# Kernel tuning notes

Measured on AMD Instinct MI355X. Metric: run time of the kernel, lower is better.

Reference implementation:

```python
import jax, jax.numpy as jnp
import numpy as np

T_STEPS = 64   # number of actions (T-1 in the torch code)
BATCH = 512
STATE = 256
ACTION = 64
BELIEF = 1024
HIDDEN = 1024
EMB = 1024
MIN_STD = 0.1


def setup_inputs() -> dict:
    key = jax.random.key(0)
    ks = jax.random.split(key, 16)
    def w(k, shape):
        return jax.random.normal(k, shape, jnp.float32) * 0.02
    return {
        "s_0": jax.random.normal(ks[0], (BATCH, STATE), jnp.float32),
        "A": jax.random.normal(ks[1], (T_STEPS, BATCH, ACTION), jnp.float32),
        "b_0": jax.random.normal(ks[2], (BATCH, BELIEF), jnp.float32),
        "O": jax.random.normal(ks[3], (T_STEPS, BATCH, EMB), jnp.float32),
        "M": jnp.ones((T_STEPS, BATCH, 1), jnp.float32),
        "noise_pri": jax.random.normal(ks[4], (T_STEPS, BATCH, STATE), jnp.float32),
        "noise_pos": jax.random.normal(ks[5], (T_STEPS, BATCH, STATE), jnp.float32),
        # learned parameters (torch nn.Linear convention: y = x @ W.T + b)
        "W_sa": w(ks[6], (BELIEF, STATE + ACTION)), "b_sa": jnp.zeros((BELIEF,), jnp.float32),
        "W_ih": w(ks[7], (3 * BELIEF, BELIEF)), "b_ih": jnp.zeros((3 * BELIEF,), jnp.float32),
        "W_hh": w(ks[8], (3 * BELIEF, BELIEF)), "b_hh": jnp.zeros((3 * BELIEF,), jnp.float32),
        "W_bpri": w(ks[9], (HIDDEN, BELIEF)), "b_bpri": jnp.zeros((HIDDEN,), jnp.float32),
        "W_spri": w(ks[10], (2 * STATE, HIDDEN)), "b_spri": jnp.zeros((2 * STATE,), jnp.float32),
        "W_bpos": w(ks[11], (HIDDEN, BELIEF + EMB)), "b_bpos": jnp.zeros((HIDDEN,), jnp.float32),
        "W_spos": w(ks[12], (2 * STATE, HIDDEN)), "b_spos": jnp.zeros((2 * STATE,), jnp.float32),
    }


def reference(s_0, A, b_0, O, M, noise_pri, noise_pos,
              W_sa, b_sa, W_ih, b_ih, W_hh, b_hh,
              W_bpri, b_bpri, W_spri, b_spri,
              W_bpos, b_bpos, W_spos, b_spos):
    act = jax.nn.relu  # cfg.activation_function = 'relu'

    def gru_cell(x, h):
        # torch GRUCell gate order: r, z, n
        gi = x @ W_ih.T + b_ih      # [B, 3*BELIEF]
        gh = h @ W_hh.T + b_hh
        i_r, i_z, i_n = jnp.split(gi, 3, axis=1)
        h_r, h_z, h_n = jnp.split(gh, 3, axis=1)
        r = jax.nn.sigmoid(i_r + h_r)
        z = jax.nn.sigmoid(i_z + h_z)
        n = jnp.tanh(i_n + r * h_n)
        return (1.0 - z) * n + z * h

    def step(carry, xs):
        b, s = carry  # belief [B,BELIEF], posterior state [B,STATE]
        a_t, o_t, m_t, eps_p, eps_q = xs
        s_in = s * m_t  # non-terminal mask
        x = act(jnp.concatenate([s_in, a_t], axis=1) @ W_sa.T + b_sa)
        b_new = gru_cell(x, b)
        # prior
        pri = act(b_new @ W_bpri.T + b_bpri) @ W_spri.T + b_spri
        mu_p, hp = jnp.split(pri, 2, axis=1)
        std_p = jax.nn.softplus(hp) + MIN_STD
        s_p = mu_p + std_p * eps_p
        # posterior (uses current observation embedding)
        pos = act(jnp.concatenate([b_new, o_t], axis=1) @ W_bpos.T + b_bpos) @ W_spos.T + b_spos
        mu_q, hq = jnp.split(pos, 2, axis=1)
        std_q = jax.nn.softplus(hq) + MIN_STD
        s_q = mu_q + std_q * eps_q
        return (b_new, s_q), (b_new, s_p, mu_p, std_p, s_q, mu_q, std_q)

    (_, _), ys = jax.lax.scan(step, (b_0, s_0), (A, O, M, noise_pri, noise_pos))
    B_out, S_pri, MU_pri, STD_pri, S_pos, MU_pos, STD_pos = ys
    return B_out, S_pri, MU_pri, STD_pri, S_pos, MU_pos, STD_pos
```

## Files before the change

kernel.cpp:

```cpp
#include <hip/hip_runtime.h>
#include <hip/hip_bf16.h>
#include <math.h>

typedef short bf16x8 __attribute__((ext_vector_type(8)));
typedef float f32x4 __attribute__((ext_vector_type(4)));
typedef unsigned short u16;

#define NT 64
#define NB 512
#define NS 256
#define NA 64
#define NBEL 1024

#define OUT_B      0
#define OUT_SPRI   33554432
#define OUT_MUPRI  41943040
#define OUT_STDPRI 50331648
#define OUT_SPOS   58720256
#define OUT_MUPOS  67108864
#define OUT_STDPOS 75497472

__device__ __forceinline__ f32x4 mfma16(bf16x8 a, bf16x8 b, f32x4 c) {
  return __builtin_amdgcn_mfma_f32_16x16x32_bf16(a, b, c, 0, 0, 0);
}

__device__ __forceinline__ u16 f2bf(float f) {
  union { float f; unsigned u; } v; v.f = f;
  return (u16)((v.u + 0x7FFFu + ((v.u >> 16) & 1u)) >> 16);
}

__device__ __forceinline__ bf16x8 ld8bf(const u16* p) { return *(const bf16x8*)p; }

__device__ __forceinline__ bf16x8 cvt8(const float* p) {
  const float4 lo = *(const float4*)p;
  const float4 hi = *(const float4*)(p + 4);
  bf16x8 v;
  v[0] = (short)f2bf(lo.x); v[1] = (short)f2bf(lo.y);
  v[2] = (short)f2bf(lo.z); v[3] = (short)f2bf(lo.w);
  v[4] = (short)f2bf(hi.x); v[5] = (short)f2bf(hi.y);
  v[6] = (short)f2bf(hi.z); v[7] = (short)f2bf(hi.w);
  return v;
}

__device__ __forceinline__ float sigm(float x) { return 1.f / (1.f + __expf(-x)); }
__device__ __forceinline__ float softplus_(float x) {
  if (x > 20.f) return x;
  return log1pf(__expf(x));
}

#define ZACC(acc) { acc[0][0] = (f32x4){0.f,0.f,0.f,0.f}; acc[0][1] = (f32x4){0.f,0.f,0.f,0.f}; \
                    acc[1][0] = (f32x4){0.f,0.f,0.f,0.f}; acc[1][1] = (f32x4){0.f,0.f,0.f,0.f}; }

#define Q4(acc, a0v, a1v, b0v, b1v) \
  acc[0][0] = mfma16(a0v, b0v, acc[0][0]); \
  acc[0][1] = mfma16(a0v, b1v, acc[0][1]); \
  acc[1][0] = mfma16(a1v, b0v, acc[1][0]); \
  acc[1][1] = mfma16(a1v, b1v, acc[1][1]);

__device__ __forceinline__ void red_write(float* L, f32x4 (&acc)[2][2], int l) {
  const int base = l * 16;
#pragma unroll
  for (int i = 0; i < 2; ++i)
#pragma unroll
    for (int j = 0; j < 2; ++j)
#pragma unroll
      for (int q = 0; q < 4; ++q)
        L[base + (i * 2 + j) * 4 + q] = acc[i][j][q];
}
__device__ __forceinline__ void red_add(const float* L, f32x4 (&acc)[2][2], int l) {
  const int base = l * 16;
#pragma unroll
  for (int i = 0; i < 2; ++i)
#pragma unroll
    for (int j = 0; j < 2; ++j)
#pragma unroll
      for (int q = 0; q < 4; ++q)
        acc[i][j][q] += L[base + (i * 2 + j) * 4 + q];
}

__global__ __launch_bounds__(256) void cvt_weights_k(
    const float* __restrict__ wsa, const float* __restrict__ wih,
    const float* __restrict__ whh, const float* __restrict__ wbpri,
    const float* __restrict__ wspri, const float* __restrict__ wbpos,
    const float* __restrict__ wspos, u16* __restrict__ dst) {
  const int S0 = 327680;
  const int S1 = S0 + 3145728;
  const int S2 = S1 + 3145728;
  const int S3 = S2 + 1048576;
  const int S4 = S3 + 524288;
  const int S5 = S4 + 2097152;
  const int S6 = S5 + 524288;
  for (int i = blockIdx.x * blockDim.x + threadIdx.x; i < S6;
       i += gridDim.x * blockDim.x) {
    float v;
    if (i < S0) v = wsa[i];
    else if (i < S1) v = wih[i - S0];
    else if (i < S2) v = whh[i - S1];
    else if (i < S3) v = wbpri[i - S2];
    else if (i < S4) v = wspri[i - S3];
    else if (i < S5) v = wbpos[i - S4];
    else v = wspos[i - S5];
    dst[i] = f2bf(v);
  }
}

__global__ __launch_bounds__(256) void init_carry_k(
    const float* __restrict__ s0, const float* __restrict__ b0,
    const float* __restrict__ Mptr, u16* __restrict__ smask,
    u16* __restrict__ bbf0, float* __restrict__ hf) {
  for (int i = blockIdx.x * blockDim.x + threadIdx.x; i < NB * NBEL;
       i += gridDim.x * blockDim.x) {
    float b = b0[i];
    bbf0[i] = f2bf(b);
    hf[i] = b;
    if (i < NB * NS) {
      int row = i >> 8;
      smask[i] = f2bf(s0[i] * Mptr[row]);
    }
  }
}

__global__ __launch_bounds__(512, 2) void kA(
    const u16* __restrict__ smask, const float* __restrict__ Af,
    const u16* __restrict__ wsa, const float* __restrict__ bsa,
    u16* __restrict__ xbf, const float* __restrict__ Of,
    const u16* __restrict__ wbpos, float* __restrict__ hbO, int t) {
  __shared__ float lred[4][1024];
  const int l = threadIdx.x & 63, r16 = l & 15, kq = l >> 4;
  const int wid8 = threadIdx.x >> 6;
  const int wid = wid8 & 3, kh = wid8 >> 2;
  if (blockIdx.x < 128) {
    const int g = blockIdx.x, bm = g >> 4, bn = g & 15;
    const int row0 = bm * 64 + (wid >> 1) * 32;
    const int col0 = bn * 64 + (wid & 1) * 32;
    f32x4 acc[2][2]; ZACC(acc);
    const u16* A0 = smask + (row0 + r16) * NS + kq * 8;
    const u16* A1 = A0 + 16 * NS;
    const u16* B0 = wsa + (size_t)(col0 + r16) * 320 + kq * 8;
    const u16* B1 = B0 + 16 * 320;
    if (kh == 0) {
#pragma unroll
      for (int k = 0; k < 160; k += 32) {
        bf16x8 a0 = ld8bf(A0 + k), a1 = ld8bf(A1 + k);
        bf16x8 b0 = ld8bf(B0 + k), b1 = ld8bf(B1 + k);
        Q4(acc, a0, a1, b0, b1);
      }
    } else {
#pragma unroll
      for (int k = 160; k < 256; k += 32) {
        bf16x8 a0 = ld8bf(A0 + k), a1 = ld8bf(A1 + k);
        bf16x8 b0 = ld8bf(B0 + k), b1 = ld8bf(B1 + k);
        Q4(acc, a0, a1, b0, b1);
      }
      const float* F0 = Af + (size_t)t * (NB * NA) + (row0 + r16) * NA + kq * 8;
      const float* F1 = F0 + 16 * NA;
      const u16* C0 = wsa + (size_t)(col0 + r16) * 320 + 256 + kq * 8;
      const u16* C1 = C0 + 16 * 320;
#pragma unroll
      for (int k = 0; k < 64; k += 32) {
        bf16x8 a0 = cvt8(F0 + k), a1 = cvt8(F1 + k);
        bf16x8 b0 = ld8bf(C0 + k), b1 = ld8bf(C1 + k);
        Q4(acc, a0, a1, b0, b1);
      }
      red_write(lred[wid], acc, l);
    }
    __syncthreads();
    if (kh == 0) {
      red_add(lred[wid], acc, l);
#pragma unroll
      for (int i = 0; i < 2; ++i)
#pragma unroll
        for (int j = 0; j < 2; ++j)
#pragma unroll
          for (int q = 0; q < 4; ++q) {
            const int row = row0 + i * 16 + kq * 4 + q;
            const int col = col0 + j * 16 + r16;
            xbf[row * NBEL + col] = f2bf(fmaxf(acc[i][j][q] + bsa[col], 0.f));
          }
    }
  } else {
    const int g = blockIdx.x - 128, bm = g >> 4, bn = g & 15;
    const int row0 = bm * 64 + (wid >> 1) * 32;
    const int col0 = bn * 64 + (wid & 1) * 32;
    f32x4 acc[2][2]; ZACC(acc);
    const float* F0 = Of + (size_t)t * (NB * NBEL) + (row0 + r16) * NBEL + kh * 512 + kq * 8;
    const float* F1 = F0 + 16 * NBEL;
    const u16* B0 = wbpos + (size_t)(col0 + r16) * 2048 + 1024 + kh * 512 + kq * 8;
    const u16* B1 = B0 + 16 * 2048;
#pragma unroll 4
    for (int k = 0; k < 512; k += 32) {
      bf16x8 a0 = cvt8(F0 + k), a1 = cvt8(F1 + k);
      bf16x8 b0 = ld8bf(B0 + k), b1 = ld8bf(B1 + k);
      Q4(acc, a0, a1, b0, b1);
    }
    if (kh == 1) red_write(lred[wid], acc, l);
    __syncthreads();
    if (kh == 0) {
      red_add(lred[wid], acc, l);
#pragma unroll
      for (int i = 0; i < 2; ++i)
#pragma unroll
        for (int j = 0; j < 2; ++j)
#pragma unroll
          for (int q = 0; q < 4; ++q) {
            const int row = row0 + i * 16 + kq * 4 + q;
            const int col = col0 + j * 16 + r16;
            hbO[row * NBEL + col] = acc[i][j][q];
          }
    }
  }
}

__global__ __launch_bounds__(512, 2) void kB(
    const u16* __restrict__ xbf, const u16* __restrict__ bprev,
    const u16* __restrict__ wih, const u16* __restrict__ whh,
    const float* __restrict__ bih, const float* __restrict__ bhh,
    float* __restrict__ hf, u16* __restrict__ bcur, float* __restrict__ out,
    const u16* __restrict__ wbpri, const float* __restrict__ bbpri,
    u16* __restrict__ hpri, int t) {
  __shared__ float lred[4][3][1024];
  const int l = threadIdx.x & 63, r16 = l & 15, kq = l >> 4;
  const int wid8 = threadIdx.x >> 6;
  const int wid = wid8 & 3, kh = wid8 >> 2;
  if (blockIdx.x < 128) {
    if (t >= NT) return;
    const int g = blockIdx.x, bm = g >> 4, bn = g & 15;
    const int row0 = bm * 64 + (wid >> 1) * 32;
    const int col0 = bn * 64 + (wid & 1) * 32;
    f32x4 ar[2][2], az[2][2], an[2][2];
    ZACC(ar); ZACC(az); ZACC(an);
    const u16* Asrc = (kh == 0) ? xbf : bprev;
    const u16* W = (kh == 0) ? wih : whh;
    const u16* A0 = Asrc + (row0 + r16) * NBEL + kq * 8;
    const u16* A1 = A0 + 16 * NBEL;
    const u16* Br0 = W + (size_t)(col0 + r16) * NBEL + kq * 8;
    const u16* Br1 = Br0 + 16 * NBEL;
    const u16* Bz0 = W + (size_t)(col0 + 1024 + r16) * NBEL + kq * 8;
    const u16* Bz1 = Bz0 + 16 * NBEL;
    const u16* Bn0 = W + (size_t)(col0 + 2048 + r16) * NBEL + kq * 8;
    const u16* Bn1 = Bn0 + 16 * NBEL;
#pragma unroll 4
    for (int k = 0; k < NBEL; k += 32) {
      bf16x8 a0 = ld8bf(A0 + k), a1 = ld8bf(A1 + k);
      bf16x8 b0 = ld8bf(Br0 + k), b1 = ld8bf(Br1 + k);
      Q4(ar, a0, a1, b0, b1);
      bf16x8 c0 = ld8bf(Bz0 + k), c1 = ld8bf(Bz1 + k);
      Q4(az, a0, a1, c0, c1);
      bf16x8 d0 = ld8bf(Bn0 + k), d1 = ld8bf(Bn1 + k);
      Q4(an, a0, a1, d0, d1);
    }
    if (kh == 1) {
      red_write(lred[wid][0], ar, l);
      red_write(lred[wid][1], az, l);
      red_write(lred[wid][2], an, l);
    }
    __syncthreads();
    if (kh == 0) {
      const int base = l * 16;
#pragma unroll
      for (int i = 0; i < 2; ++i)
#pragma unroll
        for (int j = 0; j < 2; ++j)
#pragma unroll
          for (int q = 0; q < 4; ++q) {
            const int row = row0 + i * 16 + kq * 4 + q;
            const int c = col0 + j * 16 + r16;
            const int li = base + (i * 2 + j) * 4 + q;
            const float r = sigm(ar[i][j][q] + bih[c] + lred[wid][0][li] + bhh[c]);
            const float z = sigm(az[i][j][q] + bih[c + 1024] + lred[wid][1][li] + bhh[c + 1024]);
            const float n = tanhf(an[i][j][q] + bih[c + 2048] +
                                  r * (lred[wid][2][li] + bhh[c + 2048]));
            const float h = hf[row * NBEL + c];
            const float bnew = (1.f - z) * n + z * h;
            hf[row * NBEL + c] = bnew;
            bcur[row * NBEL + c] = f2bf(bnew);
            out[OUT_B + (size_t)t * (NB * NBEL) + row * NBEL + c] = bnew;
          }
    }
  } else {
    if (t < 1) return;
    const int g = blockIdx.x - 128, bm = g >> 4, bn = g & 15;
    const int row0 = bm * 64 + (wid >> 1) * 32;
    const int col0 = bn * 64 + (wid & 1) * 32;
    f32x4 acc[2][2]; ZACC(acc);
    const u16* A0 = bprev + (row0 + r16) * NBEL + kh * 512 + kq * 8;
    const u16* A1 = A0 + 16 * NBEL;
    const u16* B0 = wbpri + (size_t)(col0 + r16) * NBEL + kh * 512 + kq * 8;
    const u16* B1 = B0 + 16 * NBEL;
#pragma unroll 4
    for (int k = 0; k < 512; k += 32) {
      bf16x8 a0 = ld8bf(A0 + k), a1 = ld8bf(A1 + k);
      bf16x8 b0 = ld8bf(B0 + k), b1 = ld8bf(B1 + k);
      Q4(acc, a0, a1, b0, b1);
    }
    if (kh == 1) red_write(lred[wid][0], acc, l);
    __syncthreads();
    if (kh == 0) {
      red_add(lred[wid][0], acc, l);
#pragma unroll
      for (int i = 0; i < 2; ++i)
#pragma unroll
        for (int j = 0; j < 2; ++j)
#pragma unroll
          for (int q = 0; q < 4; ++q) {
            const int row = row0 + i * 16 + kq * 4 + q;
            const int col = col0 + j * 16 + r16;
            hpri[row * NBEL + col] = f2bf(fmaxf(acc[i][j][q] + bbpri[col], 0.f));
          }
    }
  }
}

__global__ __launch_bounds__(512, 2) void kC(
    const u16* __restrict__ bcur, const u16* __restrict__ wbpos,
    const float* __restrict__ bbpos, const float* __restrict__ hbO,
    u16* __restrict__ hbbf,
    const u16* __restrict__ hpri, const u16* __restrict__ wspri,
    const float* __restrict__ bspri, const float* __restrict__ npri,
    float* __restrict__ out, int t) {
  __shared__ float lred[4][2][1024];
  const int l = threadIdx.x & 63, r16 = l & 15, kq = l >> 4;
  const int wid8 = threadIdx.x >> 6;
  const int wid = wid8 & 3, kh = wid8 >> 2;
  if (blockIdx.x < 128) {
    if (t >= NT) return;
    const int g = blockIdx.x, bm = g >> 4, bn = g & 15;
    const int row0 = bm * 64 + (wid >> 1) * 32;
    const int col0 = bn * 64 + (wid & 1) * 32;
    f32x4 acc[2][2]; ZACC(acc);
    const u16* A0 = bcur + (row0 + r16) * NBEL + kh * 512 + kq * 8;
    const u16* A1 = A0 + 16 * NBEL;
    const u16* B0 = wbpos + (size_t)(col0 + r16) * 2048 + kh * 512 + kq * 8;
    const u16* B1 = B0 + 16 * 2048;
#pragma unroll 4
    for (int k = 0; k < 512; k += 32) {
      bf16x8 a0 = ld8bf(A0 + k), a1 = ld8bf(A1 + k);
      bf16x8 b0 = ld8bf(B0 + k), b1 = ld8bf(B1 + k);
      Q4(acc, a0, a1, b0, b1);
    }
    if (kh == 1) red_write(lred[wid][0], acc, l);
    __syncthreads();
    if (kh == 0) {
      red_add(lred[wid][0], acc, l);
#pragma unroll
      for (int i = 0; i < 2; ++i)
#pragma unroll
        for (int j = 0; j < 2; ++j)
#pragma unroll
          for (int q = 0; q < 4; ++q) {
            const int row = row0 + i * 16 + kq * 4 + q;
            const int col = col0 + j * 16 + r16;
            const float v = acc[i][j][q] + hbO[row * NBEL + col] + bbpos[col];
            hbbf[row * NBEL + col] = f2bf(fmaxf(v, 0.f));
          }
    }
  } else {
    if (t < 1) return;
    const int g = blockIdx.x - 128, bm = g >> 2, bn = g & 3;
    const int row0 = bm * 64 + (wid >> 1) * 32;
    const int c0 = bn * 64 + (wid & 1) * 32;
    f32x4 am[2][2], ah[2][2];
    ZACC(am); ZACC(ah);
    const u16* A0 = hpri + (row0 + r16) * NBEL + kh * 512 + kq * 8;
    const u16* A1 = A0 + 16 * NBEL;
    const u16* Bm0 = wspri + (size_t)(c0 + r16) * NBEL + kh * 512 + kq * 8;
    const u16* Bm1 = Bm0 + 16 * NBEL;
    const u16* Bh0 = wspri + (size_t)(c0 + 256 + r16) * NBEL + kh * 512 + kq * 8;
    const u16* Bh1 = Bh0 + 16 * NBEL;
#pragma unroll 4
    for (int k = 0; k < 512; k += 32) {
      bf16x8 a0 = ld8bf(A0 + k), a1 = ld8bf(A1 + k);
      bf16x8 m0 = ld8bf(Bm0 + k), m1 = ld8bf(Bm1 + k);
      Q4(am, a0, a1, m0, m1);
      bf16x8 h0 = ld8bf(Bh0 + k), h1 = ld8bf(Bh1 + k);
      Q4(ah, a0, a1, h0, h1);
    }
    if (kh == 1) {
      red_write(lred[wid][0], am, l);
      red_write(lred[wid][1], ah, l);
    }
    __syncthreads();
    if (kh == 0) {
      red_add(lred[wid][0], am, l);
      red_add(lred[wid][1], ah, l);
      const int tt = t - 1;
#pragma unroll
      for (int i = 0; i < 2; ++i)
#pragma unroll
        for (int j = 0; j < 2; ++j)
#pragma unroll
          for (int q = 0; q < 4; ++q) {
            const int row = row0 + i * 16 + kq * 4 + q;
            const int c = c0 + j * 16 + r16;
            const size_t idx = (size_t)tt * (NB * NS) + row * NS + c;
            const float mu = am[i][j][q] + bspri[c];
            const float hp = ah[i][j][q] + bspri[c + 256];
            const float sd = softplus_(hp) + 0.1f;
            out[OUT_SPRI + idx] = mu + sd * npri[idx];
            out[OUT_MUPRI + idx] = mu;
            out[OUT_STDPRI + idx] = sd;
          }
    }
  }
}

__global__ __launch_bounds__(512, 2) void kD(
    const u16* __restrict__ hbbf, const u16* __restrict__ wspos,
    const float* __restrict__ bspos, const float* __restrict__ npos,
    const float* __restrict__ Mptr, float* __restrict__ out,
    u16* __restrict__ smask, int t) {
  __shared__ float lred[4][2][1024];
  const int l = threadIdx.x & 63, r16 = l & 15, kq = l >> 4;
  const int wid8 = threadIdx.x >> 6;
  const int wid = wid8 & 3, kh = wid8 >> 2;
  const int g = blockIdx.x, bm = g >> 2, bn = g & 3;
  const int row0 = bm * 64 + (wid >> 1) * 32;
  const int c0 = bn * 64 + (wid & 1) * 32;
  f32x4 am[2][2], ah[2][2];
  ZACC(am); ZACC(ah);
  const u16* A0 = hbbf + (row0 + r16) * NBEL + kh * 512 + kq * 8;
  const u16* A1 = A0 + 16 * NBEL;
  const u16* Bm0 = wspos + (size_t)(c0 + r16) * NBEL + kh * 512 + kq * 8;
  const u16* Bm1 = Bm0 + 16 * NBEL;
  const u16* Bh0 = wspos + (size_t)(c0 + 256 + r16) * NBEL + kh * 512 + kq * 8;
  const u16* Bh1 = Bh0 + 16 * NBEL;
#pragma unroll 4
  for (int k = 0; k < 512; k += 32) {
    bf16x8 a0 = ld8bf(A0 + k), a1 = ld8bf(A1 + k);
    bf16x8 m0 = ld8bf(Bm0 + k), m1 = ld8bf(Bm1 + k);
    Q4(am, a0, a1, m0, m1);
    bf16x8 h0 = ld8bf(Bh0 + k), h1 = ld8bf(Bh1 + k);
    Q4(ah, a0, a1, h0, h1);
  }
  if (kh == 1) {
    red_write(lred[wid][0], am, l);
    red_write(lred[wid][1], ah, l);
  }
  __syncthreads();
  if (kh == 0) {
    red_add(lred[wid][0], am, l);
    red_add(lred[wid][1], ah, l);
#pragma unroll
    for (int i = 0; i < 2; ++i)
#pragma unroll
      for (int j = 0; j < 2; ++j)
#pragma unroll
        for (int q = 0; q < 4; ++q) {
          const int row = row0 + i * 16 + kq * 4 + q;
          const int c = c0 + j * 16 + r16;
          const float mu = am[i][j][q] + bspos[c];
          const float hq = ah[i][j][q] + bspos[c + 256];
          const float sd = softplus_(hq) + 0.1f;
          const size_t idx = (size_t)t * (NB * NS) + row * NS + c;
          const float sq = mu + sd * npos[idx];
          out[OUT_SPOS + idx] = sq;
          out[OUT_MUPOS + idx] = mu;
          out[OUT_STDPOS + idx] = sd;
          const float mn = (t < NT - 1) ? Mptr[(t + 1) * NB + row] : 1.f;
          smask[row * NS + c] = f2bf(sq * mn);
        }
  }
}

extern "C" void kernel_launch(void* const* d_in, const int* in_sizes, int n_in,
                              void* d_out, int out_size, void* d_ws, size_t ws_size,
                              hipStream_t stream) {
  const float* s0 = (const float*)d_in[0];
  const float* Af = (const float*)d_in[1];
  const float* b0 = (const float*)d_in[2];
  const float* Of = (const float*)d_in[3];
  const float* Mp = (const float*)d_in[4];
  const float* npri = (const float*)d_in[5];
  const float* npos = (const float*)d_in[6];
  const float* Wsa = (const float*)d_in[7];
  const float* bsa = (const float*)d_in[8];
  const float* Wih = (const float*)d_in[9];
  const float* bih = (const float*)d_in[10];
  const float* Whh = (const float*)d_in[11];
  const float* bhh = (const float*)d_in[12];
  const float* Wbpri = (const float*)d_in[13];
  const float* bbpri = (const float*)d_in[14];
  const float* Wspri = (const float*)d_in[15];
  const float* bspri = (const float*)d_in[16];
  const float* Wbpos = (const float*)d_in[17];
  const float* bbpos = (const float*)d_in[18];
  const float* Wspos = (const float*)d_in[19];
  const float* bspos = (const float*)d_in[20];

  float* out = (float*)d_out;
  char* ws = (char*)d_ws;
  u16* wbase   = (u16*)ws;
  u16* wsa_b   = wbase;
  u16* wih_b   = wbase + 327680;
  u16* whh_b   = wbase + 3473408;
  u16* wbpri_b = wbase + 6619136;
  u16* wspri_b = wbase + 7667712;
  u16* wbpos_b = wbase + 8192000;
  u16* wspos_b = wbase + 10289152;
  u16*   smask = (u16*)  (ws + 21626880);
  u16*   bbf0  = (u16*)  (ws + 21889024);
  u16*   bbf1  = (u16*)  (ws + 22937600);
  float* hf    = (float*)(ws + 23986176);
  u16*   xbf   = (u16*)  (ws + 26083328);
  float* hbO   = (float*)(ws + 27131904);
  u16*   hbbf  = (u16*)  (ws + 29229056);
  u16*   hpri  = (u16*)  (ws + 30277632);

  cvt_weights_k<<<2048, 256, 0, stream>>>(Wsa, Wih, Whh, Wbpri, Wspri, Wbpos,
                                          Wspos, wbase);
  init_carry_k<<<2048, 256, 0, stream>>>(s0, b0, Mp, smask, bbf0, hf);

  for (int t = 0; t < NT; ++t) {
    const u16* bprev = (t & 1) ? bbf1 : bbf0;
    u16* bcur = (t & 1) ? bbf0 : bbf1;
    kA<<<256, 512, 0, stream>>>(smask, Af, wsa_b, bsa, xbf, Of, wbpos_b, hbO, t);
    kB<<<256, 512, 0, stream>>>(xbf, bprev, wih_b, whh_b, bih, bhh, hf, bcur,
                                out, wbpri_b, bbpri, hpri, t);
    kC<<<160, 512, 0, stream>>>(bcur, wbpos_b, bbpos, hbO, hbbf,
                                hpri, wspri_b, bspri, npri, out, t);
    kD<<<32, 512, 0, stream>>>(hbbf, wspos_b, bspos, npos, Mp, out, smask, t);
  }
  {
    const int t = NT;
    const u16* bprev = (t & 1) ? bbf1 : bbf0;
    u16* bcur = (t & 1) ? bbf0 : bbf1;
    kB<<<256, 512, 0, stream>>>(xbf, bprev, wih_b, whh_b, bih, bhh, hf, bcur,
                                out, wbpri_b, bbpri, hpri, t);
    kC<<<160, 512, 0, stream>>>(bcur, wbpos_b, bbpos, hbO, hbbf,
                                hpri, wspri_b, bspri, npri, out, t);
  }
}
```

Measured before the change: 10.06 ms.

## Replace per-step kernel launches with persistent cooperative kernel using per-XCD flag sync

Replaces the 4-launches-per-step loop with one persistent cooperative kernel of 512 blocks, partitioned by batch rows into 8 independent XCD groups. Stages within a group synchronize through atomic counters instead of kernel boundaries. This removes roughly 260 launch gaps and lets stages from adjacent steps overlap (the next observation projection, the W_hh projection for the next step). It also drops the split-K LDS reductions. Risks are spin-wait overhead, possible deadlock if not all blocks are co-resident, and different tile shapes; the old multi-launch path remains only as a fallback if the cooperative launch fails.

```diff
diff --git a/kernel.cpp b/kernel.cpp
--- a/kernel.cpp
+++ b/kernel.cpp
@@ -20,6 +20,16 @@
 #define OUT_MUPOS  67108864
 #define OUT_STDPOS 75497472
 
+#define KF_X 0
+#define KF_BPRI 1
+#define KF_HBO 2
+#define KF_G 3
+#define KF_SPRI 4
+#define KF_B 5
+#define KF_HB 6
+#define KF_GH 7
+#define KF_SMASK 8
+
 __device__ __forceinline__ f32x4 mfma16(bf16x8 a, bf16x8 b, f32x4 c) {
   return __builtin_amdgcn_mfma_f32_16x16x32_bf16(a, b, c, 0, 0, 0);
 }
@@ -27,6 +37,9 @@
 __device__ __forceinline__ u16 f2bf(float f) {
   union { float f; unsigned u; } v; v.f = f;
   return (u16)((v.u + 0x7FFFu + ((v.u >> 16) & 1u)) >> 16);
+}
+__device__ __forceinline__ float bf2f(u16 h) {
+  union { unsigned u; float f; } v; v.u = ((unsigned)h) << 16; return v.f;
 }
 
 __device__ __forceinline__ bf16x8 ld8bf(const u16* p) { return *(const bf16x8*)p; }
@@ -57,25 +70,47 @@
   acc[1][0] = mfma16(a1v, b0v, acc[1][0]); \
   acc[1][1] = mfma16(a1v, b1v, acc[1][1]);
 
-__device__ __forceinline__ void red_write(float* L, f32x4 (&acc)[2][2], int l) {
-  const int base = l * 16;
-#pragma unroll
-  for (int i = 0; i < 2; ++i)
-#pragma unroll
-    for (int j = 0; j < 2; ++j)
-#pragma unroll
-      for (int q = 0; q < 4; ++q)
-        L[base + (i * 2 + j) * 4 + q] = acc[i][j][q];
-}
-__device__ __forceinline__ void red_add(const float* L, f32x4 (&acc)[2][2], int l) {
-  const int base = l * 16;
-#pragma unroll
-  for (int i = 0; i < 2; ++i)
-#pragma unroll
-    for (int j = 0; j < 2; ++j)
-#pragma unroll
-      for (int q = 0; q < 4; ++q)
-        acc[i][j][q] += L[base + (i * 2 + j) * 4 + q];
+__device__ __forceinline__ void gtile(f32x4 (&acc)[2][2],
+    const u16* __restrict__ A, int lda, const u16* __restrict__ B, int ldb,
+    int K, int r16, int kq) {
+  const u16* A0 = A + r16 * lda + kq * 8;
+  const u16* A1 = A0 + 16 * lda;
+  const u16* B0 = B + (size_t)r16 * ldb + kq * 8;
+  const u16* B1 = B0 + 16 * ldb;
+#pragma unroll 4
+  for (int k = 0; k < K; k += 32) {
+    bf16x8 a0 = ld8bf(A0 + k), a1 = ld8bf(A1 + k);
+    bf16x8 b0 = ld8bf(B0 + k), b1 = ld8bf(B1 + k);
+    Q4(acc, a0, a1, b0, b1);
+  }
+}
+__device__ __forceinline__ void gtileF(f32x4 (&acc)[2][2],
+    const float* __restrict__ A, int lda, const u16* __restrict__ B, int ldb,
+    int K, int r16, int kq) {
+  const float* A0 = A + r16 * lda + kq * 8;
+  const float* A1 = A0 + 16 * lda;
+  const u16* B0 = B + (size_t)r16 * ldb + kq * 8;
+  const u16* B1 = B0 + 16 * ldb;
+#pragma unroll 2
+  for (int k = 0; k < K; k += 32) {
+    bf16x8 a0 = cvt8(A0 + k), a1 = cvt8(A1 + k);
+    bf16x8 b0 = ld8bf(B0 + k), b1 = ld8bf(B1 + k);
+    Q4(acc, a0, a1, b0, b1);
+  }
+}
+
+__device__ __forceinline__ void setflag(unsigned* f) {
+  __syncthreads();
+  if (threadIdx.x == 0)
+    __hip_atomic_fetch_add(f, 1u, __ATOMIC_RELEASE, __HIP_MEMORY_SCOPE_AGENT);
+}
+__device__ __forceinline__ void waitflag(unsigned* f, unsigned target) {
+  if (threadIdx.x == 0) {
+    while (__hip_atomic_load(f, __ATOMIC_RELAXED, __HIP_MEMORY_SCOPE_AGENT) < target)
+      __builtin_amdgcn_s_sleep(2);
+    (void)__hip_atomic_load(f, __ATOMIC_ACQUIRE, __HIP_MEMORY_SCOPE_AGENT);
+  }
+  __syncthreads();
 }
 
 __global__ __launch_bounds__(256) void cvt_weights_k(
@@ -102,6 +137,260 @@
     else v = wspos[i - S5];
     dst[i] = f2bf(v);
   }
+}
+
+__global__ __launch_bounds__(256) void init_scan_k(
+    const float* __restrict__ s0, const float* __restrict__ b0,
+    const float* __restrict__ Mptr, u16* __restrict__ smask,
+    u16* __restrict__ bbuf1, float* __restrict__ hf,
+    unsigned* __restrict__ flags) {
+  for (int i = blockIdx.x * blockDim.x + threadIdx.x; i < NB * NBEL;
+       i += gridDim.x * blockDim.x) {
+    const int row = i >> 10, c = i & 1023;
+    const int xcd = row >> 6, lr = row & 63;
+    const int o = xcd * 65536 + lr * 1024 + c;
+    float b = b0[i];
+    bbuf1[o] = f2bf(b);
+    hf[o] = b;
+    if (i < NB * NS) {
+      const int row2 = i >> 8, c2 = i & 255;
+      smask[(row2 >> 6) * 16384 + (row2 & 63) * 256 + c2] =
+          f2bf(s0[i] * Mptr[row2]);
+    }
+    if (i < 8 * 66 * 10) flags[i] = 0;
+  }
+}
+
+struct SP {
+  const float *Af, *Of, *Mp, *npri, *npos;
+  const float *bsa, *bih, *bhh, *bbpri, *bspri, *bbpos, *bspos;
+  const u16 *wsa, *wih, *whh, *wbpri, *wspri, *wbpos, *wspos;
+  float *out;
+  u16 *smask, *xbf, *bbuf0, *bbuf1, *gh, *hbo, *hb, *hpri;
+  float *grzn, *hf;
+  unsigned* flags;
+};
+
+__global__ void __launch_bounds__(256, 2) rssm_scan(SP p) {
+  const int xcd = blockIdx.x & 7;
+  const int s = blockIdx.x >> 3;
+  const int rb = xcd * 64;
+  const int l = threadIdx.x & 63, r16 = l & 15, kq = l >> 4;
+  const int wid = threadIdx.x >> 6;
+  const int lr0 = (wid >> 1) * 32;
+  const int lc0 = (wid & 1) * 32;
+
+  u16* smaskX = p.smask + xcd * 16384;
+  u16* xbfX   = p.xbf   + xcd * 65536;
+  float* grznX = p.grzn + xcd * 196608;
+  u16* bbufX[2] = {p.bbuf0 + xcd * 65536, p.bbuf1 + xcd * 65536};
+  float* hfX  = p.hf    + xcd * 65536;
+  u16* ghX    = p.gh    + xcd * 196608;
+  u16* hboX   = p.hbo   + xcd * 131072;
+  u16* hbX    = p.hb    + xcd * 65536;
+  u16* hpriX  = p.hpri  + xcd * 65536;
+  unsigned* F = p.flags + xcd * 660;
+#define FLG(t, k) (F + (t) * 10 + (k))
+
+#define EPI(body) _Pragma("unroll") for (int i = 0; i < 2; ++i) \
+  _Pragma("unroll") for (int j = 0; j < 2; ++j) \
+  _Pragma("unroll") for (int q = 0; q < 4; ++q) { \
+    const int lrow = lr0 + i * 16 + kq * 4 + q; \
+    const int jc = j * 16 + r16; \
+    body }
+
+  if (s < 16) {
+    const int colw = s * 64 + lc0;
+    f32x4 acc[2][2]; ZACC(acc);
+    gtileF(acc, p.Of + (size_t)(rb + lr0) * NBEL, NBEL,
+           p.wbpos + (size_t)colw * 2048 + 1024, 2048, 1024, r16, kq);
+    EPI({ hboX[lrow * 1024 + colw + jc] = f2bf(acc[i][j][q]); })
+    setflag(FLG(0, KF_HBO));
+  } else {
+    const int colw = (s - 16) * 64 + lc0;
+    f32x4 acc[2][2]; ZACC(acc);
+    gtile(acc, bbufX[1] + lr0 * 1024, 1024,
+          p.whh + (size_t)colw * 1024, 1024, 1024, r16, kq);
+    EPI({ const int c = colw + jc;
+          ghX[lrow * 3072 + c] = f2bf(acc[i][j][q] + p.bhh[c]); })
+    setflag(FLG(0, KF_GH));
+  }
+
+  for (int t = 0; t <= NT; ++t) {
+    u16* bcur = bbufX[t & 1];
+    const u16* bprev = bbufX[(t & 1) ^ 1];
+
+    if (s < 16) {
+      if (t < NT) {
+        if (t > 0) waitflag(FLG(t, KF_SMASK), 4);
+        const int colw = s * 64 + lc0;
+        f32x4 acc[2][2]; ZACC(acc);
+        gtile(acc, smaskX + lr0 * 256, 256,
+              p.wsa + (size_t)colw * 320, 320, 256, r16, kq);
+        gtileF(acc, p.Af + (size_t)t * (NB * NA) + (size_t)(rb + lr0) * NA, NA,
+               p.wsa + (size_t)colw * 320 + 256, 320, 64, r16, kq);
+        EPI({ const int c = colw + jc;
+              xbfX[lrow * 1024 + c] = f2bf(fmaxf(acc[i][j][q] + p.bsa[c], 0.f)); })
+        setflag(FLG(t, KF_X));
+      }
+    } else if (s < 32) {
+      if (t >= 1) {
+        waitflag(FLG(t - 1, KF_B), 8);
+        if (t >= 2) waitflag(FLG(t - 1, KF_SPRI), 4);
+        const int colw = (s - 16) * 64 + lc0;
+        f32x4 acc[2][2]; ZACC(acc);
+        gtile(acc, bprev + lr0 * 1024, 1024,
+              p.wbpri + (size_t)colw * 1024, 1024, 1024, r16, kq);
+        EPI({ const int c = colw + jc;
+              hpriX[lrow * 1024 + c] = f2bf(fmaxf(acc[i][j][q] + p.bbpri[c], 0.f)); })
+        setflag(FLG(t, KF_BPRI));
+      }
+    } else if (s < 48) {
+      if (t + 1 < NT) {
+        if (t >= 1) waitflag(FLG(t - 1, KF_HB), 16);
+        const int colw = (s - 32) * 64 + lc0;
+        f32x4 acc[2][2]; ZACC(acc);
+        gtileF(acc, p.Of + (size_t)(t + 1) * (NB * NBEL) + (size_t)(rb + lr0) * NBEL,
+               NBEL, p.wbpos + (size_t)colw * 2048 + 1024, 2048, 1024, r16, kq);
+        u16* dst = hboX + ((t + 1) & 1) * 65536;
+        EPI({ dst[lrow * 1024 + colw + jc] = f2bf(acc[i][j][q]); })
+        setflag(FLG(t + 1, KF_HBO));
+      }
+    }
+
+    if (s < 48) {
+      if (t < NT) {
+        waitflag(FLG(t, KF_X), 16);
+        const int G = s / 16;
+        const int colw = (s % 16) * 64 + lc0;
+        f32x4 acc[2][2]; ZACC(acc);
+        gtile(acc, xbfX + lr0 * 1024, 1024,
+              p.wih + ((size_t)(G << 10) + colw) * 1024, 1024, 1024, r16, kq);
+        EPI({ const int c = colw + jc;
+              grznX[lrow * 3072 + (G << 10) + c] = acc[i][j][q] + p.bih[(G << 10) + c]; })
+        setflag(FLG(t, KF_G));
+      }
+    } else if (s < 52) {
+      if (t >= 1) {
+        waitflag(FLG(t, KF_BPRI), 16);
+        const int colw = (s - 48) * 64 + lc0;
+        f32x4 am[2][2], ah[2][2]; ZACC(am); ZACC(ah);
+        gtile(am, hpriX + lr0 * 1024, 1024,
+              p.wspri + (size_t)colw * 1024, 1024, 1024, r16, kq);
+        gtile(ah, hpriX + lr0 * 1024, 1024,
+              p.wspri + (size_t)(256 + colw) * 1024, 1024, 1024, r16, kq);
+        const int tt = t - 1;
+        EPI({ const int c = colw + jc;
+              const size_t idx = (size_t)tt * (NB * NS) + (size_t)(rb + lrow) * NS + c;
+              const float mu = am[i][j][q] + p.bspri[c];
+              const float hp = ah[i][j][q] + p.bspri[c + 256];
+              const float sd = softplus_(hp) + 0.1f;
+              p.out[OUT_SPRI + idx] = mu + sd * p.npri[idx];
+              p.out[OUT_MUPRI + idx] = mu;
+              p.out[OUT_STDPRI + idx] = sd; })
+        setflag(FLG(t, KF_SPRI));
+      }
+    }
+
+    if (s >= 56 && t < NT) {
+      waitflag(FLG(t, KF_G), 48);
+      waitflag(FLG(t, KF_GH), 48);
+      const int ce = (s - 56) * 128;
+      const int row = threadIdx.x >> 2;
+      const int cbase = ce + (threadIdx.x & 3) * 32;
+      const float* gi = grznX + row * 3072;
+      const u16* ghr = ghX + row * 3072;
+      float* hrow = hfX + row * 1024;
+      u16* brow = bcur + row * 1024;
+      float* orow = p.out + OUT_B + (size_t)t * (NB * NBEL) + (size_t)(rb + row) * NBEL;
+#pragma unroll 8
+      for (int ii = 0; ii < 32; ++ii) {
+        const int c = cbase + ii;
+        const float r = sigm(gi[c] + bf2f(ghr[c]));
+        const float z = sigm(gi[c + 1024] + bf2f(ghr[c + 1024]));
+        const float n = tanhf(gi[c + 2048] + r * bf2f(ghr[c + 2048]));
+        const float h = hrow[c];
+        const float bnew = (1.f - z) * n + z * h;
+        hrow[c] = bnew;
+        brow[c] = f2bf(bnew);
+        orow[c] = bnew;
+      }
+      setflag(FLG(t, KF_B));
+    }
+
+    if (s < 16) {
+      if (t < NT) {
+        waitflag(FLG(t, KF_B), 8);
+        waitflag(FLG(t, KF_HBO), 16);
+        const int colw = s * 64 + lc0;
+        f32x4 acc[2][2]; ZACC(acc);
+        gtile(acc, bcur + lr0 * 1024, 1024,
+              p.wbpos + (size_t)colw * 2048, 2048, 1024, r16, kq);
+        const u16* ho = hboX + (t & 1) * 65536;
+        EPI({ const int c = colw + jc;
+              const float v = acc[i][j][q] + bf2f(ho[lrow * 1024 + c]) + p.bbpos[c];
+              hbX[lrow * 1024 + c] = f2bf(fmaxf(v, 0.f)); })
+        setflag(FLG(t, KF_HB));
+      }
+    } else {
+      if (t + 1 < NT) {
+        waitflag(FLG(t, KF_B), 8);
+        const int colw = (s - 16) * 64 + lc0;
+        f32x4 acc[2][2]; ZACC(acc);
+        gtile(acc, bcur + lr0 * 1024, 1024,
+              p.whh + (size_t)colw * 1024, 1024, 1024, r16, kq);
+        EPI({ const int c = colw + jc;
+              ghX[lrow * 3072 + c] = f2bf(acc[i][j][q] + p.bhh[c]); })
+        setflag(FLG(t + 1, KF_GH));
+      }
+    }
+
+    if (s < 4 && t < NT) {
+      waitflag(FLG(t, KF_HB), 16);
+      const int colw = s * 64 + lc0;
+      f32x4 am[2][2], ah[2][2]; ZACC(am); ZACC(ah);
+      gtile(am, hbX + lr0 * 1024, 1024,
+            p.wspos + (size_t)colw * 1024, 1024, 1024, r16, kq);
+      gtile(ah, hbX + lr0 * 1024, 1024,
+            p.wspos + (size_t)(256 + colw) * 1024, 1024, 1024, r16, kq);
+      EPI({ const int c = colw + jc;
+            const int rg = rb + lrow;
+            const size_t idx = (size_t)t * (NB * NS) + (size_t)rg * NS + c;
+            const float mu = am[i][j][q] + p.bspos[c];
+            const float hq = ah[i][j][q] + p.bspos[c + 256];
+            const float sd = softplus_(hq) + 0.1f;
+            const float sq = mu + sd * p.npos[idx];
+            p.out[OUT_SPOS + idx] = sq;
+            p.out[OUT_MUPOS + idx] = mu;
+            p.out[OUT_STDPOS + idx] = sd;
+            const float mn = (t < NT - 1) ? p.Mp[(t + 1) * NB + rg] : 1.f;
+            smaskX[lrow * 256 + c] = f2bf(sq * mn); })
+      setflag(FLG(t + 1, KF_SMASK));
+    }
+  }
+#undef FLG
+#undef EPI
+}
+
+__device__ __forceinline__ void red_write(float* L, f32x4 (&acc)[2][2], int l) {
+  const int base = l * 16;
+#pragma unroll
+  for (int i = 0; i < 2; ++i)
+#pragma unroll
+    for (int j = 0; j < 2; ++j)
+#pragma unroll
+      for (int q = 0; q < 4; ++q)
+        L[base + (i * 2 + j) * 4 + q] = acc[i][j][q];
+}
+__device__ __forceinline__ void red_add(const float* L, f32x4 (&acc)[2][2], int l) {
+  const int base = l * 16;
+#pragma unroll
+  for (int i = 0; i < 2; ++i)
+#pragma unroll
+    for (int j = 0; j < 2; ++j)
+#pragma unroll
+      for (int q = 0; q < 4; ++q)
+        acc[i][j][q] += L[base + (i * 2 + j) * 4 + q];
 }
 
 __global__ __launch_bounds__(256) void init_carry_k(
@@ -250,9 +539,9 @@
       Q4(an, a0, a1, d0, d1);
     }
     if (kh == 1) {
-      red_write(lred[wid][0], ar, l);
-      red_write(lred[wid][1], az, l);
-      red_write(lred[wid][2], an, l);
+      red_write(&lred[wid][0][0], ar, l);
+      red_write(&lred[wid][1][0], az, l);
+      red_write(&lred[wid][2][0], an, l);
     }
     __syncthreads();
     if (kh == 0) {
@@ -293,10 +582,10 @@
       bf16x8 b0 = ld8bf(B0 + k), b1 = ld8bf(B1 + k);
       Q4(acc, a0, a1, b0, b1);
     }
-    if (kh == 1) red_write(lred[wid][0], acc, l);
+    if (kh == 1) red_write(&lred[wid][0][0], acc, l);
     __syncthreads();
     if (kh == 0) {
-      red_add(lred[wid][0], acc, l);
+      red_add(&lred[wid][0][0], acc, l);
 #pragma unroll
       for (int i = 0; i < 2; ++i)
 #pragma unroll
@@ -338,10 +627,10 @@
       bf16x8 b0 = ld8bf(B0 + k), b1 = ld8bf(B1 + k);
       Q4(acc, a0, a1, b0, b1);
     }
-    if (kh == 1) red_write(lred[wid][0], acc, l);
+    if (kh == 1) red_write(&lred[wid][0][0], acc, l);
     __syncthreads();
     if (kh == 0) {
-      red_add(lred[wid][0], acc, l);
+      red_add(&lred[wid][0][0], acc, l);
 #pragma unroll
       for (int i = 0; i < 2; ++i)
 #pragma unroll
@@ -376,13 +665,13 @@
       Q4(ah, a0, a1, h0, h1);
     }
     if (kh == 1) {
-      red_write(lred[wid][0], am, l);
-      red_write(lred[wid][1], ah, l);
+      red_write(&lred[wid][0][0], am, l);
+      red_write(&lred[wid][1][0], ah, l);
     }
     __syncthreads();
     if (kh == 0) {
-      red_add(lred[wid][0], am, l);
-      red_add(lred[wid][1], ah, l);
+      red_add(&lred[wid][0][0], am, l);
+      red_add(&lred[wid][1][0], ah, l);
       const int tt = t - 1;
 #pragma unroll
       for (int i = 0; i < 2; ++i)
@@ -433,13 +722,13 @@
     Q4(ah, a0, a1, h0, h1);
   }
   if (kh == 1) {
-    red_write(lred[wid][0], am, l);
-    red_write(lred[wid][1], ah, l);
+    red_write(&lred[wid][0][0], am, l);
+    red_write(&lred[wid][1][0], ah, l);
   }
   __syncthreads();
   if (kh == 0) {
-    red_add(lred[wid][0], am, l);
-    red_add(lred[wid][1], ah, l);
+    red_add(&lred[wid][0][0], am, l);
+    red_add(&lred[wid][1][0], ah, l);
 #pragma unroll
     for (int i = 0; i < 2; ++i)
 #pragma unroll
@@ -497,6 +786,41 @@
   u16* wspri_b = wbase + 7667712;
   u16* wbpos_b = wbase + 8192000;
   u16* wspos_b = wbase + 10289152;
+
+  unsigned* flags = (unsigned*)(ws + 21626880);
+  u16*   smaskC = (u16*)  (ws + 21659648);
+  u16*   xbfC   = (u16*)  (ws + 21921792);
+  float* grznC  = (float*)(ws + 22970368);
+  u16*   bbuf0C = (u16*)  (ws + 29261824);
+  u16*   bbuf1C = (u16*)  (ws + 30310400);
+  float* hfC    = (float*)(ws + 31358976);
+  u16*   ghC    = (u16*)  (ws + 33456128);
+  u16*   hboC   = (u16*)  (ws + 36601856);
+  u16*   hbC    = (u16*)  (ws + 38699008);
+  u16*   hpriC  = (u16*)  (ws + 39747584);
+
+  cvt_weights_k<<<2048, 256, 0, stream>>>(Wsa, Wih, Whh, Wbpri, Wspri, Wbpos,
+                                          Wspos, wbase);
+  init_scan_k<<<2048, 256, 0, stream>>>(s0, b0, Mp, smaskC, bbuf1C, hfC, flags);
+
+  SP p;
+  p.Af = Af; p.Of = Of; p.Mp = Mp; p.npri = npri; p.npos = npos;
+  p.bsa = bsa; p.bih = bih; p.bhh = bhh; p.bbpri = bbpri; p.bspri = bspri;
+  p.bbpos = bbpos; p.bspos = bspos;
+  p.wsa = wsa_b; p.wih = wih_b; p.whh = whh_b; p.wbpri = wbpri_b;
+  p.wspri = wspri_b; p.wbpos = wbpos_b; p.wspos = wspos_b;
+  p.out = out;
+  p.smask = smaskC; p.xbf = xbfC; p.bbuf0 = bbuf0C; p.bbuf1 = bbuf1C;
+  p.gh = ghC; p.hbo = hboC; p.hb = hbC; p.hpri = hpriC;
+  p.grzn = grznC; p.hf = hfC;
+  p.flags = flags;
+
+  void* args[] = {(void*)&p};
+  hipError_t err = hipLaunchCooperativeKernel(
+      reinterpret_cast<const void*>(&rssm_scan), dim3(512), dim3(256),
+      args, 0, stream);
+  if (err == hipSuccess) return;
+
   u16*   smask = (u16*)  (ws + 21626880);
   u16*   bbf0  = (u16*)  (ws + 21889024);
   u16*   bbf1  = (u16*)  (ws + 22937600);
@@ -506,10 +830,7 @@
   u16*   hbbf  = (u16*)  (ws + 29229056);
   u16*   hpri  = (u16*)  (ws + 30277632);
 
-  cvt_weights_k<<<2048, 256, 0, stream>>>(Wsa, Wih, Whh, Wbpri, Wspri, Wbpos,
-                                          Wspos, wbase);
   init_carry_k<<<2048, 256, 0, stream>>>(s0, b0, Mp, smask, bbf0, hf);
-
   for (int t = 0; t < NT; ++t) {
     const u16* bprev = (t & 1) ? bbf1 : bbf0;
     u16* bcur = (t & 1) ? bbf0 : bbf1;
```

Result: slower. 16.34 ms (+62.4%).
